# Kernel tuning notes

Measured on AMD Instinct MI355X. Metric: run time of the kernel, lower is better.

## Reference

```python
import jax, jax.numpy as jnp
import numpy as np

NUM_EMBEDDINGS = 1024
EMBEDDING_DIM = 64
COMMITMENT_COST = 0.1
DECAY = 0.9
EPSILON = 1e-05


def setup_inputs() -> dict:
    key = jax.random.key(0)
    k1, k2, k3 = jax.random.split(key, 3)
    inputs = jax.random.normal(k1, (16, EMBEDDING_DIM, 4096), dtype=jnp.float32)
    embedding_weight = jax.random.normal(k2, (NUM_EMBEDDINGS, EMBEDDING_DIM), dtype=jnp.float32)
    ema_cluster_size = jnp.zeros((NUM_EMBEDDINGS,), dtype=jnp.float32)
    ema_w = jax.random.normal(k3, (NUM_EMBEDDINGS, EMBEDDING_DIM), dtype=jnp.float32)
    return {
        "inputs": inputs,
        "embedding_weight": embedding_weight,
        "ema_cluster_size": ema_cluster_size,
        "ema_w": ema_w,
    }


def reference(inputs, embedding_weight, ema_cluster_size, ema_w):
    K, D = embedding_weight.shape
    # (B, C, L) -> (B, L, C); C == embedding_dim
    x = jnp.transpose(inputs, (0, 2, 1))
    B, L, _ = x.shape
    flat = x.reshape(-1, D)  # [N, D], N = B*L
    N = flat.shape[0]

    distances = (
        jnp.sum(flat * flat, axis=1, keepdims=True)
        + jnp.sum(embedding_weight * embedding_weight, axis=1)
        - 2.0 * (flat @ embedding_weight.T)
    )
    idx = jnp.argmin(distances, axis=1)  # [N] int

    # embedding lookup (equivalent to one-hot @ weight)
    quantized = embedding_weight[idx].reshape(B, L, D)

    # one-hot column sums and scatter-reduction, without materializing [N, K]
    counts = jnp.zeros((K,), dtype=flat.dtype).at[idx].add(1.0)  # sum(encodings, 0)
    dw = jax.ops.segment_sum(flat, idx, num_segments=K)  # encodings^T @ flat_input

    # EMA updates (training path)
    cs = ema_cluster_size * DECAY + (1.0 - DECAY) * counts
    n = jnp.sum(cs)
    cs = (cs + EPSILON) / (n + K * EPSILON) * n
    new_ema_w = ema_w * DECAY + (1.0 - DECAY) * dw
    new_embedding_weight = new_ema_w / cs[:, None]

    # KLDivLoss(batchmean)(softmax(quantized.detach()), softmax(inputs)) over dim=2
    p_in = jax.nn.softmax(jax.lax.stop_gradient(quantized), axis=2)
    p_tgt = jax.nn.softmax(x, axis=2)
    kl = jnp.sum(p_tgt * (jnp.log(p_tgt) - p_in)) / B
    loss = COMMITMENT_COST * kl

    # straight-through estimator
    quantized_st = x + jax.lax.stop_gradient(quantized - x)

    avg_probs = counts / N
    perplexity = jnp.exp(-jnp.sum(avg_probs * jnp.log(avg_probs + 1e-10)))

    out = jnp.transpose(quantized_st, (0, 2, 1))  # back to (B, C, L)
    encoding_indices = idx[:, None]
    return (out, loss, perplexity, new_embedding_weight, encoding_indices)
```

## Files before the change

kernel.cpp:

```cpp
#include <hip/hip_runtime.h>

#define LDIM 4096
#define DDIM 64
#define KCODES 1024
#define BDIM 16
#define NROWS 65536
#define NSLICE 8
#define SLICE_ROWS (NROWS / NSLICE)

typedef __attribute__((ext_vector_type(8))) short short8;
typedef __attribute__((ext_vector_type(16))) float float16v;

__device__ __forceinline__ unsigned int orderf(float f) {
  unsigned int u = __float_as_uint(f);
  return (u & 0x80000000u) ? ~u : (u | 0x80000000u);
}

__device__ __forceinline__ unsigned long long shfl_xor_u64(unsigned long long v, int m) {
  int lo = __shfl_xor((int)(unsigned int)(v & 0xffffffffull), m, 64);
  int hi = __shfl_xor((int)(unsigned int)(v >> 32), m, 64);
  return ((unsigned long long)(unsigned int)hi << 32) | (unsigned int)lo;
}

__device__ __forceinline__ unsigned int bf16_rne(float x) {
  unsigned int u = __float_as_uint(x);
  return (u + 0x7FFFu + ((u >> 16) & 1u)) >> 16;
}

__global__ void prep_kernel(const float* __restrict__ Ew,
                            float* __restrict__ enorm,
                            float* __restrict__ SE,
                            unsigned short* __restrict__ Epk2) {
  int k = blockIdx.x;
  int d = threadIdx.x;
  float v = Ew[k * DDIM + d];
  float n2 = v * v;
  #pragma unroll
  for (int o = 32; o > 0; o >>= 1) n2 += __shfl_xor(n2, o, 64);
  float m = v;
  #pragma unroll
  for (int o = 32; o > 0; o >>= 1) m = fmaxf(m, __shfl_xor(m, o, 64));
  float e = __expf(v - m);
  float Z = e;
  #pragma unroll
  for (int o = 32; o > 0; o >>= 1) Z += __shfl_xor(Z, o, 64);
  SE[k * DDIM + d] = e / Z;
  if (d == 0) enorm[k] = n2;

  unsigned int rh = bf16_rne(v);
  float hif = __uint_as_float(rh << 16);
  unsigned int rl = bf16_rne(v - hif);
  int tile = k >> 5, mm = k & 31;
  int s = d >> 4, h = (d >> 3) & 1, j = d & 7;
  int base = tile * 4096 + (h * 32 + mm) * 8 + j;
  Epk2[base + s * 512]        = (unsigned short)rh;
  Epk2[base + (4 + s) * 512]  = (unsigned short)rl;
}

__launch_bounds__(256, 2)
__global__ void argmin_kernel(const float* __restrict__ inp,
                              const unsigned short* __restrict__ Epk2,
                              const float* __restrict__ enorm,
                              int* __restrict__ idx_ws,
                              float* __restrict__ outidx) {
  const int tid = threadIdx.x;
  const int lane = tid & 63;
  const int w = tid >> 6;
  const int half = lane >> 5;
  const int m = lane & 31;
  const int row_base = blockIdx.x * 128 + w * 32;
  const int b = row_base >> 12;
  const int l0 = row_base & 4095;
  const float* xp = inp + (size_t)b * DDIM * LDIM + l0 + m;

  short8 afr[8];
  #pragma unroll
  for (int s = 0; s < 4; s++) {
    #pragma unroll
    for (int j = 0; j < 8; j++) {
      int d = 16 * s + 8 * half + j;
      float x = xp[(size_t)d * LDIM];
      unsigned int rh = bf16_rne(x);
      float hif = __uint_as_float(rh << 16);
      unsigned int rl = bf16_rne(x - hif);
      afr[s][j] = (short)(unsigned short)rh;
      afr[4 + s][j] = (short)(unsigned short)rl;
    }
  }

  float bsc[16];
  int bix[16];
  #pragma unroll
  for (int j = 0; j < 16; j++) { bsc[j] = 1e30f; bix[j] = 0; }

  const unsigned short* eb = Epk2 + lane * 8;

  short8 bA[8], bB[8];
  float enA, enB;

  #pragma unroll
  for (int s = 0; s < 4; s++) {
    bA[s]     = *(const short8*)(eb + s * 512);
    bA[4 + s] = *(const short8*)(eb + 2048 + s * 512);
  }
  enA = enorm[m];

  #pragma unroll 1
  for (int i = 0; i < 16; i++) {
    const int tB = 2 * i + 1;
    {
      const unsigned short* p = eb + tB * 4096;
      #pragma unroll
      for (int s = 0; s < 4; s++) {
        bB[s]     = *(const short8*)(p + s * 512);
        bB[4 + s] = *(const short8*)(p + 2048 + s * 512);
      }
      enB = enorm[tB * 32 + m];
    }
    {
      float16v a0 = {}, a1 = {}, a2 = {};
      #pragma unroll
      for (int s = 0; s < 4; s++) {
        a0 = __builtin_amdgcn_mfma_f32_32x32x16_bf16(afr[s], bA[s], a0, 0, 0, 0);
        a1 = __builtin_amdgcn_mfma_f32_32x32x16_bf16(afr[s], bA[4 + s], a1, 0, 0, 0);
        a2 = __builtin_amdgcn_mfma_f32_32x32x16_bf16(afr[4 + s], bA[s], a2, 0, 0, 0);
      }
      int ci = 2 * i * 32 + m;
      #pragma unroll
      for (int j = 0; j < 16; j++) {
        float sc = fmaf(-2.f, a0[j] + a1[j] + a2[j], enA);
        if (sc < bsc[j]) { bsc[j] = sc; bix[j] = ci; }
      }
    }
    if (i < 15) {
      const unsigned short* p = eb + (2 * i + 2) * 4096;
      #pragma unroll
      for (int s = 0; s < 4; s++) {
        bA[s]     = *(const short8*)(p + s * 512);
        bA[4 + s] = *(const short8*)(p + 2048 + s * 512);
      }
      enA = enorm[(2 * i + 2) * 32 + m];
    }
    {
      float16v a0 = {}, a1 = {}, a2 = {};
      #pragma unroll
      for (int s = 0; s < 4; s++) {
        a0 = __builtin_amdgcn_mfma_f32_32x32x16_bf16(afr[s], bB[s], a0, 0, 0, 0);
        a1 = __builtin_amdgcn_mfma_f32_32x32x16_bf16(afr[s], bB[4 + s], a1, 0, 0, 0);
        a2 = __builtin_amdgcn_mfma_f32_32x32x16_bf16(afr[4 + s], bB[s], a2, 0, 0, 0);
      }
      int ci = tB * 32 + m;
      #pragma unroll
      for (int j = 0; j < 16; j++) {
        float sc = fmaf(-2.f, a0[j] + a1[j] + a2[j], enB);
        if (sc < bsc[j]) { bsc[j] = sc; bix[j] = ci; }
      }
    }
  }

  #pragma unroll
  for (int j = 0; j < 16; j++) {
    unsigned long long key =
        ((unsigned long long)orderf(bsc[j]) << 32) | (unsigned int)bix[j];
    #pragma unroll
    for (int mm = 1; mm < 32; mm <<= 1) {
      unsigned long long o = shfl_xor_u64(key, mm);
      if (o < key) key = o;
    }
    if (m == 0) {
      int row_local = (j & 3) + 8 * (j >> 2) + 4 * half;
      int grow = row_base + row_local;
      int cidx = (int)(key & 0xffffffffull);
      idx_ws[grow] = cidx;
      outidx[grow] = (float)cidx;
    }
  }
}

__launch_bounds__(256)
__global__ void out_kl_kernel(const float* __restrict__ inp,
                              const float* __restrict__ Ew,
                              const float* __restrict__ SE,
                              const int* __restrict__ idx_ws,
                              float* __restrict__ out,
                              float* __restrict__ klacc) {
  __shared__ float Zs[4][64], S1s[4][64], Us[4][64];
  const int tid = threadIdx.x;
  const int c = tid >> 6;
  const int i = tid & 63;
  const int r = blockIdx.x * 64 + i;
  const int b = r >> 12, l = r & 4095;
  const float* xp = inp + (size_t)b * DDIM * LDIM + l;
  float* op = out + (size_t)b * DDIM * LDIM + l;
  const int k = idx_ws[r];
  const float4* Ek4 = (const float4*)(Ew + k * DDIM) + c * 4;
  const float4* Qk4 = (const float4*)(SE + k * DDIM) + c * 4;

  float Z = 0.f, S1 = 0.f, U = 0.f;
  #pragma unroll
  for (int t = 0; t < 4; t++) {
    float ek[4], qk[4];
    *(float4*)ek = Ek4[t];
    *(float4*)qk = Qk4[t];
    #pragma unroll
    for (int u = 0; u < 4; u++) {
      int d = c * 16 + t * 4 + u;
      float x = xp[(size_t)d * LDIM];
      float e = __expf(x);
      Z += e;
      S1 += e * x;
      U += e * qk[u];
      op[(size_t)d * LDIM] = ek[u];
    }
  }
  Zs[c][i] = Z; S1s[c][i] = S1; Us[c][i] = U;
  __syncthreads();
  if (tid < 64) {
    float Zt = Zs[0][i] + Zs[1][i] + Zs[2][i] + Zs[3][i];
    float S1t = S1s[0][i] + S1s[1][i] + S1s[2][i] + S1s[3][i];
    float Ut = Us[0][i] + Us[1][i] + Us[2][i] + Us[3][i];
    float kl = (S1t - Ut) / Zt - __logf(Zt);
    #pragma unroll
    for (int o = 32; o > 0; o >>= 1) kl += __shfl_xor(kl, o, 64);
    if (i == 0) atomicAdd(klacc, kl);
  }
}

__launch_bounds__(512)
__global__ void dw_partial_kernel(const float* __restrict__ inp,
                                  const int* __restrict__ idx_ws,
                                  float* __restrict__ partial,
                                  float* __restrict__ pcounts) {
  __shared__ float dwp[KCODES];
  __shared__ float cnt[KCODES];
  const int d = blockIdx.x & 63;
  const int slice = blockIdx.x >> 6;
  const int tid = threadIdx.x;
  const bool do_cnt = (d == 0);

  #pragma unroll
  for (int i = 0; i < KCODES / 512; i++) {
    dwp[tid + i * 512] = 0.f;
    cnt[tid + i * 512] = 0.f;
  }
  __syncthreads();

  const int r0 = slice * SLICE_ROWS;
  for (int i = tid; i < SLICE_ROWS; i += 512) {
    int r = r0 + i;
    int b = r >> 12, l = r & 4095;
    float x = inp[(size_t)b * DDIM * LDIM + (size_t)d * LDIM + l];
    int k = idx_ws[r];
    atomicAdd(&dwp[k], x);
    if (do_cnt) atomicAdd(&cnt[k], 1.0f);
  }
  __syncthreads();

  float* dst = partial + ((size_t)slice * 64 + d) * KCODES;
  #pragma unroll
  for (int i = 0; i < KCODES / 512; i++) dst[tid + i * 512] = dwp[tid + i * 512];
  if (do_cnt) {
    float* cd = pcounts + (size_t)slice * KCODES;
    #pragma unroll
    for (int i = 0; i < KCODES / 512; i++) cd[tid + i * 512] = cnt[tid + i * 512];
  }
}

__global__ void csp_kernel(const float* __restrict__ ema_cs,
                           const float* __restrict__ pcounts,
                           float* __restrict__ csp,
                           float* __restrict__ perp_out) {
  __shared__ float red1[16], red2[16];
  int k = threadIdx.x;
  float c = 0.f;
  #pragma unroll
  for (int sl = 0; sl < NSLICE; sl++) c += pcounts[sl * KCODES + k];
  float cs = ema_cs[k] * 0.9f + 0.1f * c;
  float n = cs;
  #pragma unroll
  for (int o = 32; o > 0; o >>= 1) n += __shfl_xor(n, o, 64);
  if ((k & 63) == 0) red1[k >> 6] = n;
  float a = c * (1.0f / 65536.0f);
  float ent = a * logf(a + 1e-10f);
  float es = ent;
  #pragma unroll
  for (int o = 32; o > 0; o >>= 1) es += __shfl_xor(es, o, 64);
  if ((k & 63) == 0) red2[k >> 6] = es;
  __syncthreads();
  if (k == 0) {
    float t1 = 0.f, t2 = 0.f;
    for (int i = 0; i < 16; i++) { t1 += red1[i]; t2 += red2[i]; }
    red1[0] = t1;
    *perp_out = expf(-t2);
  }
  __syncthreads();
  float N = red1[0];
  csp[k] = (cs + 1e-5f) / (N + 1024.0f * 1e-5f) * N;
}

__launch_bounds__(256)
__global__ void reduce_embed_kernel(const float* __restrict__ partial,
                                    const float* __restrict__ emaw,
                                    const float* __restrict__ csp,
                                    const float* __restrict__ klacc,
                                    float* __restrict__ emb_out,
                                    float* __restrict__ loss_out) {
  int i = blockIdx.x * 256 + threadIdx.x;
  int k = i >> 6, d = i & 63;
  float s = 0.f;
  #pragma unroll
  for (int sl = 0; sl < NSLICE; sl++)
    s += partial[((size_t)sl * 64 + d) * KCODES + k];
  float v = fmaf(0.1f, s, emaw[i] * 0.9f);
  emb_out[i] = v / csp[k];
  if (i == 0) *loss_out = 0.1f * (*klacc) * (1.0f / 16.0f);
}

extern "C" void kernel_launch(void* const* d_in, const int* in_sizes, int n_in,
                              void* d_out, int out_size, void* d_ws, size_t ws_size,
                              hipStream_t stream) {
  const float* inp   = (const float*)d_in[0];
  const float* Ew    = (const float*)d_in[1];
  const float* emacs = (const float*)d_in[2];
  const float* emaw  = (const float*)d_in[3];

  float* out      = (float*)d_out;
  float* loss_out = out + 4194304;
  float* perp_out = out + 4194305;
  float* emb_out  = out + 4194306;
  float* idxf_out = out + 4194306 + 65536;

  char* ws = (char*)d_ws;
  int*   idx_ws  = (int*)(ws);
  float* klacc   = (float*)(ws + 262144);
  float* enorm   = (float*)(ws + 266496);
  float* csp     = (float*)(ws + 270592);
  float* SE      = (float*)(ws + 274688);
  unsigned short* Epk2 = (unsigned short*)(ws + 536832);
  float* partial = (float*)(ws + 536832);
  float* pcounts = (float*)(ws + 2633984);

  hipMemsetAsync(ws + 262144, 0, 256, stream);

  prep_kernel<<<KCODES, 64, 0, stream>>>(Ew, enorm, SE, Epk2);
  argmin_kernel<<<512, 256, 0, stream>>>(inp, Epk2, enorm, idx_ws, idxf_out);
  dw_partial_kernel<<<64 * NSLICE, 512, 0, stream>>>(inp, idx_ws, partial, pcounts);
  csp_kernel<<<1, 1024, 0, stream>>>(emacs, pcounts, csp, perp_out);
  out_kl_kernel<<<NROWS / 64, 256, 0, stream>>>(inp, Ew, SE, idx_ws, out, klacc);
  reduce_embed_kernel<<<NROWS / 256, 256, 0, stream>>>(partial, emaw, csp, klacc,
                                                       emb_out, loss_out);
}
```

Measured before the change: 178.8 us.

## Merge out/KL and dw-partial kernels into one launch, fold csp into finalize

Runs the output/KL pass and the per-dimension scatter-sum pass as two block ranges of a single kernel launch, so both independent workloads share the GPU instead of running back to back. The separate single-block csp kernel is removed. The total N is computed algebraically as 0.9·sum(ema_cs)+0.1·NROWS, and the perplexity and loss are handled by block 0 of the finalize kernel. This saves two launches and lets the streaming and atomic-heavy work overlap. In exchange the dw blocks use 256 threads instead of 512 and the shared LDS size is padded to the larger layout.

Measured after the change: 164.1 us. -8.2%, faster.

```diff
diff --git a/kernel.cpp b/kernel.cpp
--- a/kernel.cpp
+++ b/kernel.cpp
@@ -178,142 +178,152 @@
 }
 
 __launch_bounds__(256)
-__global__ void out_kl_kernel(const float* __restrict__ inp,
-                              const float* __restrict__ Ew,
-                              const float* __restrict__ SE,
-                              const int* __restrict__ idx_ws,
-                              float* __restrict__ out,
-                              float* __restrict__ klacc) {
-  __shared__ float Zs[4][64], S1s[4][64], Us[4][64];
+__global__ void outkl_dw_kernel(const float* __restrict__ inp,
+                                const float* __restrict__ Ew,
+                                const float* __restrict__ SE,
+                                const int* __restrict__ idx_ws,
+                                float* __restrict__ out,
+                                float* __restrict__ klacc,
+                                float* __restrict__ partial,
+                                float* __restrict__ pcounts) {
+  __shared__ float lds[2 * KCODES];
   const int tid = threadIdx.x;
-  const int c = tid >> 6;
-  const int i = tid & 63;
-  const int r = blockIdx.x * 64 + i;
-  const int b = r >> 12, l = r & 4095;
-  const float* xp = inp + (size_t)b * DDIM * LDIM + l;
-  float* op = out + (size_t)b * DDIM * LDIM + l;
-  const int k = idx_ws[r];
-  const float4* Ek4 = (const float4*)(Ew + k * DDIM) + c * 4;
-  const float4* Qk4 = (const float4*)(SE + k * DDIM) + c * 4;
-
-  float Z = 0.f, S1 = 0.f, U = 0.f;
-  #pragma unroll
-  for (int t = 0; t < 4; t++) {
-    float ek[4], qk[4];
-    *(float4*)ek = Ek4[t];
-    *(float4*)qk = Qk4[t];
-    #pragma unroll
-    for (int u = 0; u < 4; u++) {
-      int d = c * 16 + t * 4 + u;
-      float x = xp[(size_t)d * LDIM];
-      float e = __expf(x);
-      Z += e;
-      S1 += e * x;
-      U += e * qk[u];
-      op[(size_t)d * LDIM] = ek[u];
-    }
-  }
-  Zs[c][i] = Z; S1s[c][i] = S1; Us[c][i] = U;
+
+  if (blockIdx.x < 1024) {
+    float* Zs  = lds;
+    float* S1s = lds + 256;
+    float* Us  = lds + 512;
+    const int c = tid >> 6;
+    const int i = tid & 63;
+    const int r = blockIdx.x * 64 + i;
+    const int b = r >> 12, l = r & 4095;
+    const float* xp = inp + (size_t)b * DDIM * LDIM + l;
+    float* op = out + (size_t)b * DDIM * LDIM + l;
+    const int k = idx_ws[r];
+    const float4* Ek4 = (const float4*)(Ew + k * DDIM) + c * 4;
+    const float4* Qk4 = (const float4*)(SE + k * DDIM) + c * 4;
+
+    float Z = 0.f, S1 = 0.f, U = 0.f;
+    #pragma unroll
+    for (int t = 0; t < 4; t++) {
+      float ek[4], qk[4];
+      *(float4*)ek = Ek4[t];
+      *(float4*)qk = Qk4[t];
+      #pragma unroll
+      for (int u = 0; u < 4; u++) {
+        int d = c * 16 + t * 4 + u;
+        float x = xp[(size_t)d * LDIM];
+        float e = __expf(x);
+        Z += e;
+        S1 += e * x;
+        U += e * qk[u];
+        op[(size_t)d * LDIM] = ek[u];
+      }
+    }
+    Zs[c * 64 + i] = Z; S1s[c * 64 + i] = S1; Us[c * 64 + i] = U;
+    __syncthreads();
+    if (tid < 64) {
+      float Zt = Zs[i] + Zs[64 + i] + Zs[128 + i] + Zs[192 + i];
+      float S1t = S1s[i] + S1s[64 + i] + S1s[128 + i] + S1s[192 + i];
+      float Ut = Us[i] + Us[64 + i] + Us[128 + i] + Us[192 + i];
+      float kl = (S1t - Ut) / Zt - __logf(Zt);
+      #pragma unroll
+      for (int o = 32; o > 0; o >>= 1) kl += __shfl_xor(kl, o, 64);
+      if (i == 0) atomicAdd(klacc, kl);
+    }
+  } else {
+    float* dwp = lds;
+    float* cnt = lds + KCODES;
+    const int bid = blockIdx.x - 1024;
+    const int d = bid & 63;
+    const int slice = bid >> 6;
+    const bool do_cnt = (d == 0);
+
+    #pragma unroll
+    for (int i = 0; i < KCODES / 256; i++) {
+      dwp[tid + i * 256] = 0.f;
+      cnt[tid + i * 256] = 0.f;
+    }
+    __syncthreads();
+
+    const int r0 = slice * SLICE_ROWS;
+    for (int i = tid; i < SLICE_ROWS; i += 256) {
+      int r = r0 + i;
+      int b = r >> 12, l = r & 4095;
+      float x = inp[(size_t)b * DDIM * LDIM + (size_t)d * LDIM + l];
+      int k = idx_ws[r];
+      atomicAdd(&dwp[k], x);
+      if (do_cnt) atomicAdd(&cnt[k], 1.0f);
+    }
+    __syncthreads();
+
+    float* dst = partial + ((size_t)slice * 64 + d) * KCODES;
+    #pragma unroll
+    for (int i = 0; i < KCODES / 256; i++) dst[tid + i * 256] = dwp[tid + i * 256];
+    if (do_cnt) {
+      float* cd = pcounts + (size_t)slice * KCODES;
+      #pragma unroll
+      for (int i = 0; i < KCODES / 256; i++) cd[tid + i * 256] = cnt[tid + i * 256];
+    }
+  }
+}
+
+__launch_bounds__(256)
+__global__ void finalize_kernel(const float* __restrict__ partial,
+                                const float* __restrict__ pcounts,
+                                const float* __restrict__ emaw,
+                                const float* __restrict__ emacs,
+                                const float* __restrict__ klacc,
+                                float* __restrict__ emb_out,
+                                float* __restrict__ loss_out,
+                                float* __restrict__ perp_out) {
+  __shared__ float red[4], red2[4];
+  const int tid = threadIdx.x;
+  const int i = blockIdx.x * 256 + tid;
+  const int k = i >> 6, d = i & 63;
+
+  float se = 0.f;
+  #pragma unroll
+  for (int t = 0; t < 4; t++) se += emacs[tid * 4 + t];
+  #pragma unroll
+  for (int o = 32; o > 0; o >>= 1) se += __shfl_xor(se, o, 64);
+  if ((tid & 63) == 0) red[tid >> 6] = se;
   __syncthreads();
-  if (tid < 64) {
-    float Zt = Zs[0][i] + Zs[1][i] + Zs[2][i] + Zs[3][i];
-    float S1t = S1s[0][i] + S1s[1][i] + S1s[2][i] + S1s[3][i];
-    float Ut = Us[0][i] + Us[1][i] + Us[2][i] + Us[3][i];
-    float kl = (S1t - Ut) / Zt - __logf(Zt);
-    #pragma unroll
-    for (int o = 32; o > 0; o >>= 1) kl += __shfl_xor(kl, o, 64);
-    if (i == 0) atomicAdd(klacc, kl);
-  }
-}
-
-__launch_bounds__(512)
-__global__ void dw_partial_kernel(const float* __restrict__ inp,
-                                  const int* __restrict__ idx_ws,
-                                  float* __restrict__ partial,
-                                  float* __restrict__ pcounts) {
-  __shared__ float dwp[KCODES];
-  __shared__ float cnt[KCODES];
-  const int d = blockIdx.x & 63;
-  const int slice = blockIdx.x >> 6;
-  const int tid = threadIdx.x;
-  const bool do_cnt = (d == 0);
-
-  #pragma unroll
-  for (int i = 0; i < KCODES / 512; i++) {
-    dwp[tid + i * 512] = 0.f;
-    cnt[tid + i * 512] = 0.f;
-  }
-  __syncthreads();
-
-  const int r0 = slice * SLICE_ROWS;
-  for (int i = tid; i < SLICE_ROWS; i += 512) {
-    int r = r0 + i;
-    int b = r >> 12, l = r & 4095;
-    float x = inp[(size_t)b * DDIM * LDIM + (size_t)d * LDIM + l];
-    int k = idx_ws[r];
-    atomicAdd(&dwp[k], x);
-    if (do_cnt) atomicAdd(&cnt[k], 1.0f);
-  }
-  __syncthreads();
-
-  float* dst = partial + ((size_t)slice * 64 + d) * KCODES;
-  #pragma unroll
-  for (int i = 0; i < KCODES / 512; i++) dst[tid + i * 512] = dwp[tid + i * 512];
-  if (do_cnt) {
-    float* cd = pcounts + (size_t)slice * KCODES;
-    #pragma unroll
-    for (int i = 0; i < KCODES / 512; i++) cd[tid + i * 512] = cnt[tid + i * 512];
-  }
-}
-
-__global__ void csp_kernel(const float* __restrict__ ema_cs,
-                           const float* __restrict__ pcounts,
-                           float* __restrict__ csp,
-                           float* __restrict__ perp_out) {
-  __shared__ float red1[16], red2[16];
-  int k = threadIdx.x;
+  const float S = red[0] + red[1] + red[2] + red[3];
+  const float N = 0.9f * S + 0.1f * (float)NROWS;
+
   float c = 0.f;
   #pragma unroll
   for (int sl = 0; sl < NSLICE; sl++) c += pcounts[sl * KCODES + k];
-  float cs = ema_cs[k] * 0.9f + 0.1f * c;
-  float n = cs;
-  #pragma unroll
-  for (int o = 32; o > 0; o >>= 1) n += __shfl_xor(n, o, 64);
-  if ((k & 63) == 0) red1[k >> 6] = n;
-  float a = c * (1.0f / 65536.0f);
-  float ent = a * logf(a + 1e-10f);
-  float es = ent;
-  #pragma unroll
-  for (int o = 32; o > 0; o >>= 1) es += __shfl_xor(es, o, 64);
-  if ((k & 63) == 0) red2[k >> 6] = es;
-  __syncthreads();
-  if (k == 0) {
-    float t1 = 0.f, t2 = 0.f;
-    for (int i = 0; i < 16; i++) { t1 += red1[i]; t2 += red2[i]; }
-    red1[0] = t1;
-    *perp_out = expf(-t2);
-  }
-  __syncthreads();
-  float N = red1[0];
-  csp[k] = (cs + 1e-5f) / (N + 1024.0f * 1e-5f) * N;
-}
-
-__launch_bounds__(256)
-__global__ void reduce_embed_kernel(const float* __restrict__ partial,
-                                    const float* __restrict__ emaw,
-                                    const float* __restrict__ csp,
-                                    const float* __restrict__ klacc,
-                                    float* __restrict__ emb_out,
-                                    float* __restrict__ loss_out) {
-  int i = blockIdx.x * 256 + threadIdx.x;
-  int k = i >> 6, d = i & 63;
+  float cs = fmaf(0.1f, c, emacs[k] * 0.9f);
+  float csp = (cs + 1e-5f) / (N + (float)KCODES * 1e-5f) * N;
+
   float s = 0.f;
   #pragma unroll
   for (int sl = 0; sl < NSLICE; sl++)
     s += partial[((size_t)sl * 64 + d) * KCODES + k];
-  float v = fmaf(0.1f, s, emaw[i] * 0.9f);
-  emb_out[i] = v / csp[k];
-  if (i == 0) *loss_out = 0.1f * (*klacc) * (1.0f / 16.0f);
+  emb_out[i] = fmaf(0.1f, s, emaw[i] * 0.9f) / csp;
+
+  if (blockIdx.x == 0) {
+    float es = 0.f;
+    #pragma unroll
+    for (int t = 0; t < 4; t++) {
+      int kk = tid * 4 + t;
+      float cc = 0.f;
+      #pragma unroll
+      for (int sl = 0; sl < NSLICE; sl++) cc += pcounts[sl * KCODES + kk];
+      float a = cc * (1.0f / (float)NROWS);
+      es += a * logf(a + 1e-10f);
+    }
+    #pragma unroll
+    for (int o = 32; o > 0; o >>= 1) es += __shfl_xor(es, o, 64);
+    if ((tid & 63) == 0) red2[tid >> 6] = es;
+    __syncthreads();
+    if (tid == 0) {
+      *perp_out = expf(-(red2[0] + red2[1] + red2[2] + red2[3]));
+      *loss_out = 0.1f * (*klacc) * (1.0f / 16.0f);
+    }
+  }
 }
 
 extern "C" void kernel_launch(void* const* d_in, const int* in_sizes, int n_in,
@@ -334,7 +344,6 @@
   int*   idx_ws  = (int*)(ws);
   float* klacc   = (float*)(ws + 262144);
   float* enorm   = (float*)(ws + 266496);
-  float* csp     = (float*)(ws + 270592);
   float* SE      = (float*)(ws + 274688);
   unsigned short* Epk2 = (unsigned short*)(ws + 536832);
   float* partial = (float*)(ws + 536832);
@@ -344,9 +353,9 @@
 
   prep_kernel<<<KCODES, 64, 0, stream>>>(Ew, enorm, SE, Epk2);
   argmin_kernel<<<512, 256, 0, stream>>>(inp, Epk2, enorm, idx_ws, idxf_out);
-  dw_partial_kernel<<<64 * NSLICE, 512, 0, stream>>>(inp, idx_ws, partial, pcounts);
-  csp_kernel<<<1, 1024, 0, stream>>>(emacs, pcounts, csp, perp_out);
-  out_kl_kernel<<<NROWS / 64, 256, 0, stream>>>(inp, Ew, SE, idx_ws, out, klacc);
-  reduce_embed_kernel<<<NROWS / 256, 256, 0, stream>>>(partial, emaw, csp, klacc,
-                                                       emb_out, loss_out);
-}
+  outkl_dw_kernel<<<1536, 256, 0, stream>>>(inp, Ew, SE, idx_ws, out, klacc,
+                                            partial, pcounts);
+  finalize_kernel<<<NROWS / 256, 256, 0, stream>>>(partial, pcounts, emaw, emacs,
+                                                   klacc, emb_out, loss_out,
+                                                   perp_out);
+}
```
